# Kernel tuning notes

Hardware: AMD Instinct MI355X
Metric: run time of the kernel (lower is better)

The kernel has to match this reference:

```python
import jax, jax.numpy as jnp
import numpy as np

B, CI, H, W = 16, 32, 224, 224
CO, K, STRIDE = 32, 3, 1


def setup_inputs() -> dict:
    key = jax.random.key(0)
    k1, k2, k3 = jax.random.split(key, 3)
    x = jax.random.normal(k1, (B, CI, H, W), dtype=jnp.float32)
    weights = jax.random.normal(k2, (CO, CI, K, K), dtype=jnp.float32)
    bias = jax.random.normal(k3, (CO,), dtype=jnp.float32)
    return {"x": x, "weights": weights, "bias": bias}


def reference(x, weights, bias):
    # Faithful to HandmadeConv2D with padding=0, stride=1: a VALID
    # cross-correlation (the torch code never actually pads x) plus bias.
    out = jax.lax.conv_general_dilated(
        x, weights,
        window_strides=(STRIDE, STRIDE),
        padding="VALID",
        dimension_numbers=("NCHW", "OIHW", "NCHW"),
    )
    return out + bias[None, :, None, None]
```

## Files before the change

kernel.cpp:

```cpp
#include <hip/hip_runtime.h>
#include <hip/hip_bf16.h>

#define B_   16
#define CI_  32
#define H_   224
#define W_   224
#define CO_  32
#define OH_  222
#define OW_  222
#define HW_  (H_*W_)
#define K_   288

#define OWTW   64
#define PXT_   66
#define NPAIR  33
#define RING   10
#define SLABB  (PXT_*CI_*2)
#define CHROWS 20
#define NCHUNK 12
#define NBLK   (NCHUNK*4*B_)

typedef __attribute__((ext_vector_type(8))) short short8;
typedef __attribute__((ext_vector_type(4))) float float4v;
typedef float float4u __attribute__((ext_vector_type(4), aligned(4)));

__device__ __forceinline__ unsigned swz(unsigned L) {
    return L ^ (((L >> 7) & 7u) << 4);
}

__device__ __forceinline__ int wrap10(int v) {
    if (v >= 20) return v - 20;
    if (v >= 10) return v - 10;
    return v;
}

__global__ void wprep(const float* __restrict__ w, unsigned short* __restrict__ wbf) {
    int idx = blockIdx.x * 256 + threadIdx.x;
    if (idx >= CO_ * K_) return;
    int co  = idx / K_;
    int rem = idx - co * K_;
    int ci  = rem / 9;
    int g   = rem - ci * 9;
    unsigned int u = __float_as_uint(w[idx]);
    u = u + 0x7FFFu + ((u >> 16) & 1u);
    wbf[co * K_ + g * 32 + ci] = (unsigned short)(u >> 16);
}

__device__ __forceinline__ void load_pair(const float* __restrict__ xp, int c, float2* f2) {
    if (c + 1 < W_) {
#pragma unroll
        for (int i = 0; i < 32; ++i)
            f2[i] = *(const float2*)&xp[(size_t)i * HW_ + c];
    } else {
#pragma unroll
        for (int i = 0; i < 32; ++i) {
            float v = xp[(size_t)i * HW_ + (W_ - 1)];
            f2[i] = make_float2(v, v);
        }
    }
}

__device__ __forceinline__ void cvt_write_pair(unsigned short* Xs, int slot, int j,
                                               const float2* f2) {
    union { short8 s8[8]; __hip_bfloat162 h2[32]; } u;
#pragma unroll
    for (int i = 0; i < 16; ++i) {
        u.h2[i]      = __float22bfloat162_rn(make_float2(f2[2*i].x, f2[2*i+1].x));
        u.h2[16 + i] = __float22bfloat162_rn(make_float2(f2[2*i].y, f2[2*i+1].y));
    }
    const unsigned base = (unsigned)(slot * NPAIR + j) * 128u;
#pragma unroll
    for (int k = 0; k < 8; ++k)
        *(short8*)((char*)Xs + swz(base + (unsigned)k * 16u)) = u.s8[k];
}

__global__ __launch_bounds__(256, 3) void conv_fused(
    const float* __restrict__ x, const unsigned short* __restrict__ wbf,
    const float* __restrict__ bias, float* __restrict__ out)
{
    __shared__ unsigned short Xs[RING * PXT_ * CI_];

    const int t   = threadIdx.x;
    const int bid = blockIdx.x;
    const int xcd   = bid & 7;
    const int owt   = (bid >> 3) & 3;
    const int gid   = (bid >> 5) * 8 + xcd;
    const int b     = gid / NCHUNK;
    const int chunk = gid - b * NCHUNK;
    const int r0    = chunk * CHROWS;
    const int ow0   = owt * OWTW;
    const int NS    = min(5, (OH_ - r0 + 3) >> 2);

    const int lane = t & 63, wv = t >> 6;
    const int i16  = lane & 15, quad = lane >> 4;

    const float* xb = x + (size_t)b * CI_ * HW_;

    float2 f2[32];

    if (t < 6 * NPAIR) {
        const int tr = t / NPAIR, j = t - tr * NPAIR;
        int gr = r0 + tr; if (gr > H_ - 1) gr = H_ - 1;
        load_pair(xb + (size_t)gr * W_, ow0 + 2 * j, f2);
        cvt_write_pair(Xs, tr, j, f2);
    }
    __syncthreads();

    const float bv0 = bias[i16];
    const float bv1 = bias[16 + i16];
    const unsigned short* wr0 = wbf + (size_t)i16 * K_;
    const unsigned short* wr1 = wbf + (size_t)(16 + i16) * K_;

    const int s_tr = t / NPAIR;
    const int s_j  = t - s_tr * NPAIR;
    const int s_c  = ow0 + 2 * s_j;

    for (int s = 0; s < NS; ++s) {
        const bool pref = (t < 4 * NPAIR) && (s + 1 < NS);
        int slotW = 0;
        if (pref) {
            const int gr0 = r0 + 4 * s + 6 + s_tr;
            slotW = wrap10(4 * s + 6 + s_tr);
            const int gr = gr0 > H_ - 1 ? H_ - 1 : gr0;
            load_pair(xb + (size_t)gr * W_, s_c, f2);
        }
        __builtin_amdgcn_sched_barrier(0);

        const int oh = r0 + 4 * s + wv;
        if (oh < OH_) {
            float4v acc[4][2] = {};
            const int sl0 = 4 * s + wv;
#pragma unroll
            for (int g = 0; g < 9; ++g) {
                const int kh = g / 3, kw = g - kh * 3;
                const int sl = wrap10(sl0 + kh);
                const short8 b0 = *(const short8*)&wr0[g * 32 + quad * 8];
                const short8 b1 = *(const short8*)&wr1[g * 32 + quad * 8];
                const unsigned rowbase = (unsigned)(sl * SLABB) + (unsigned)quad * 16u;
#pragma unroll
                for (int ot = 0; ot < 4; ++ot) {
                    const unsigned L = rowbase + (unsigned)(ot * 16 + i16 + kw) * 64u;
                    const short8 a = *(const short8*)((const char*)Xs + swz(L));
                    acc[ot][0] = __builtin_amdgcn_mfma_f32_16x16x32_bf16(a, b0, acc[ot][0], 0, 0, 0);
                    acc[ot][1] = __builtin_amdgcn_mfma_f32_16x16x32_bf16(a, b1, acc[ot][1], 0, 0, 0);
                }
            }
            const size_t o0 = ((size_t)(b * CO_ + i16) * OH_ + oh) * (size_t)OW_;
            const size_t o1 = ((size_t)(b * CO_ + 16 + i16) * OH_ + oh) * (size_t)OW_;
#pragma unroll
            for (int ot = 0; ot < 4; ++ot) {
                const int owq = ow0 + ot * 16 + quad * 4;
                float4u v0 = { acc[ot][0][0] + bv0, acc[ot][0][1] + bv0,
                               acc[ot][0][2] + bv0, acc[ot][0][3] + bv0 };
                float4u v1 = { acc[ot][1][0] + bv1, acc[ot][1][1] + bv1,
                               acc[ot][1][2] + bv1, acc[ot][1][3] + bv1 };
                if (owq + 3 < OW_) {
                    *(float4u*)&out[o0 + owq] = v0;
                    *(float4u*)&out[o1 + owq] = v1;
                } else {
#pragma unroll
                    for (int r = 0; r < 4; ++r)
                        if (owq + r < OW_) {
                            out[o0 + owq + r] = acc[ot][0][r] + bv0;
                            out[o1 + owq + r] = acc[ot][1][r] + bv1;
                        }
                }
            }
        }

        if (pref) cvt_write_pair(Xs, slotW, s_j, f2);
        __syncthreads();
    }
}

extern "C" void kernel_launch(void* const* d_in, const int* in_sizes, int n_in,
                              void* d_out, int out_size, void* d_ws, size_t ws_size,
                              hipStream_t stream) {
    const float* x    = (const float*)d_in[0];
    const float* w    = (const float*)d_in[1];
    const float* bias = (const float*)d_in[2];
    float* out        = (float*)d_out;
    unsigned short* wbf = (unsigned short*)d_ws;

    wprep<<<(CO_ * K_ + 255) / 256, 256, 0, stream>>>(w, wbf);
    conv_fused<<<dim3(NBLK), 256, 0, stream>>>(x, wbf, bias, out);
}
```

Measured before the change: 233.9 us.

## Double threads per block, splitting channel loads and output tiles across waves

Moves from 256 to 512 threads per block. Each loader thread now fetches half of the 32 input channels (16 float2 values instead of 32), which halves register pressure from the prefetch buffer. Each of the 8 waves computes two 16-column output tiles instead of four. The goal is more memory-level parallelism and more resident waves (launch bounds 512,6) to hide global load latency. The cost is that per-wave weight fragment loads are duplicated and there are more threads per barrier.

```diff
diff --git a/kernel.cpp b/kernel.cpp
--- a/kernel.cpp
+++ b/kernel.cpp
@@ -19,6 +19,8 @@
 #define CHROWS 20
 #define NCHUNK 12
 #define NBLK   (NCHUNK*4*B_)
+#define STG    264
+#define PRO    396
 
 typedef __attribute__((ext_vector_type(8))) short short8;
 typedef __attribute__((ext_vector_type(4))) float float4v;
@@ -46,35 +48,38 @@
     wbf[co * K_ + g * 32 + ci] = (unsigned short)(u >> 16);
 }
 
-__device__ __forceinline__ void load_pair(const float* __restrict__ xp, int c, float2* f2) {
+__device__ __forceinline__ void load_half(const float* __restrict__ xp, int c, int h,
+                                          float2* f2) {
+    const float* p = xp + (size_t)(h * 16) * HW_;
     if (c + 1 < W_) {
 #pragma unroll
-        for (int i = 0; i < 32; ++i)
-            f2[i] = *(const float2*)&xp[(size_t)i * HW_ + c];
+        for (int i = 0; i < 16; ++i)
+            f2[i] = *(const float2*)&p[(size_t)i * HW_ + c];
     } else {
 #pragma unroll
-        for (int i = 0; i < 32; ++i) {
-            float v = xp[(size_t)i * HW_ + (W_ - 1)];
+        for (int i = 0; i < 16; ++i) {
+            float v = p[(size_t)i * HW_ + (W_ - 1)];
             f2[i] = make_float2(v, v);
         }
     }
 }
 
-__device__ __forceinline__ void cvt_write_pair(unsigned short* Xs, int slot, int j,
+__device__ __forceinline__ void cvt_write_half(unsigned short* Xs, int slot, int j, int h,
                                                const float2* f2) {
-    union { short8 s8[8]; __hip_bfloat162 h2[32]; } u;
-#pragma unroll
-    for (int i = 0; i < 16; ++i) {
-        u.h2[i]      = __float22bfloat162_rn(make_float2(f2[2*i].x, f2[2*i+1].x));
-        u.h2[16 + i] = __float22bfloat162_rn(make_float2(f2[2*i].y, f2[2*i+1].y));
+    union { short8 s8[4]; __hip_bfloat162 h2[16]; } u;
+#pragma unroll
+    for (int i = 0; i < 8; ++i) {
+        u.h2[i]     = __float22bfloat162_rn(make_float2(f2[2*i].x, f2[2*i+1].x));
+        u.h2[8 + i] = __float22bfloat162_rn(make_float2(f2[2*i].y, f2[2*i+1].y));
     }
     const unsigned base = (unsigned)(slot * NPAIR + j) * 128u;
-#pragma unroll
-    for (int k = 0; k < 8; ++k)
-        *(short8*)((char*)Xs + swz(base + (unsigned)k * 16u)) = u.s8[k];
-}
-
-__global__ __launch_bounds__(256, 3) void conv_fused(
+    *(short8*)((char*)Xs + swz(base + (unsigned)(2*h)     * 16u)) = u.s8[0];
+    *(short8*)((char*)Xs + swz(base + (unsigned)(2*h + 1) * 16u)) = u.s8[1];
+    *(short8*)((char*)Xs + swz(base + (unsigned)(4 + 2*h) * 16u)) = u.s8[2];
+    *(short8*)((char*)Xs + swz(base + (unsigned)(5 + 2*h) * 16u)) = u.s8[3];
+}
+
+__global__ __launch_bounds__(512, 6) void conv_fused(
     const float* __restrict__ x, const unsigned short* __restrict__ wbf,
     const float* __restrict__ bias, float* __restrict__ out)
 {
@@ -96,13 +101,15 @@
 
     const float* xb = x + (size_t)b * CI_ * HW_;
 
-    float2 f2[32];
-
-    if (t < 6 * NPAIR) {
-        const int tr = t / NPAIR, j = t - tr * NPAIR;
+    float2 f2[16];
+
+    if (t < PRO) {
+        const int h  = t & 1;
+        const int pj = t >> 1;
+        const int tr = pj / NPAIR, j = pj - tr * NPAIR;
         int gr = r0 + tr; if (gr > H_ - 1) gr = H_ - 1;
-        load_pair(xb + (size_t)gr * W_, ow0 + 2 * j, f2);
-        cvt_write_pair(Xs, tr, j, f2);
+        load_half(xb + (size_t)gr * W_, ow0 + 2 * j, h, f2);
+        cvt_write_half(Xs, tr, j, h, f2);
     }
     __syncthreads();
 
@@ -111,25 +118,30 @@
     const unsigned short* wr0 = wbf + (size_t)i16 * K_;
     const unsigned short* wr1 = wbf + (size_t)(16 + i16) * K_;
 
-    const int s_tr = t / NPAIR;
-    const int s_j  = t - s_tr * NPAIR;
+    const int s_h  = t & 1;
+    const int s_pj = t >> 1;
+    const int s_tr = s_pj / NPAIR;
+    const int s_j  = s_pj - s_tr * NPAIR;
     const int s_c  = ow0 + 2 * s_j;
 
+    const int row = wv >> 1;
+    const int oth = wv & 1;
+
     for (int s = 0; s < NS; ++s) {
-        const bool pref = (t < 4 * NPAIR) && (s + 1 < NS);
+        const bool pref = (t < STG) && (s + 1 < NS);
         int slotW = 0;
         if (pref) {
             const int gr0 = r0 + 4 * s + 6 + s_tr;
             slotW = wrap10(4 * s + 6 + s_tr);
             const int gr = gr0 > H_ - 1 ? H_ - 1 : gr0;
-            load_pair(xb + (size_t)gr * W_, s_c, f2);
+            load_half(xb + (size_t)gr * W_, s_c, s_h, f2);
         }
         __builtin_amdgcn_sched_barrier(0);
 
-        const int oh = r0 + 4 * s + wv;
+        const int oh = r0 + 4 * s + row;
         if (oh < OH_) {
-            float4v acc[4][2] = {};
-            const int sl0 = 4 * s + wv;
+            float4v acc[2][2] = {};
+            const int sl0 = 4 * s + row;
 #pragma unroll
             for (int g = 0; g < 9; ++g) {
                 const int kh = g / 3, kw = g - kh * 3;
@@ -138,22 +150,24 @@
                 const short8 b1 = *(const short8*)&wr1[g * 32 + quad * 8];
                 const unsigned rowbase = (unsigned)(sl * SLABB) + (unsigned)quad * 16u;
 #pragma unroll
-                for (int ot = 0; ot < 4; ++ot) {
+                for (int oti = 0; oti < 2; ++oti) {
+                    const int ot = 2 * oth + oti;
                     const unsigned L = rowbase + (unsigned)(ot * 16 + i16 + kw) * 64u;
                     const short8 a = *(const short8*)((const char*)Xs + swz(L));
-                    acc[ot][0] = __builtin_amdgcn_mfma_f32_16x16x32_bf16(a, b0, acc[ot][0], 0, 0, 0);
-                    acc[ot][1] = __builtin_amdgcn_mfma_f32_16x16x32_bf16(a, b1, acc[ot][1], 0, 0, 0);
+                    acc[oti][0] = __builtin_amdgcn_mfma_f32_16x16x32_bf16(a, b0, acc[oti][0], 0, 0, 0);
+                    acc[oti][1] = __builtin_amdgcn_mfma_f32_16x16x32_bf16(a, b1, acc[oti][1], 0, 0, 0);
                 }
             }
             const size_t o0 = ((size_t)(b * CO_ + i16) * OH_ + oh) * (size_t)OW_;
             const size_t o1 = ((size_t)(b * CO_ + 16 + i16) * OH_ + oh) * (size_t)OW_;
 #pragma unroll
-            for (int ot = 0; ot < 4; ++ot) {
+            for (int oti = 0; oti < 2; ++oti) {
+                const int ot  = 2 * oth + oti;
                 const int owq = ow0 + ot * 16 + quad * 4;
-                float4u v0 = { acc[ot][0][0] + bv0, acc[ot][0][1] + bv0,
-                               acc[ot][0][2] + bv0, acc[ot][0][3] + bv0 };
-                float4u v1 = { acc[ot][1][0] + bv1, acc[ot][1][1] + bv1,
-                               acc[ot][1][2] + bv1, acc[ot][1][3] + bv1 };
+                float4u v0 = { acc[oti][0][0] + bv0, acc[oti][0][1] + bv0,
+                               acc[oti][0][2] + bv0, acc[oti][0][3] + bv0 };
+                float4u v1 = { acc[oti][1][0] + bv1, acc[oti][1][1] + bv1,
+                               acc[oti][1][2] + bv1, acc[oti][1][3] + bv1 };
                 if (owq + 3 < OW_) {
                     *(float4u*)&out[o0 + owq] = v0;
                     *(float4u*)&out[o1 + owq] = v1;
@@ -161,14 +175,14 @@
 #pragma unroll
                     for (int r = 0; r < 4; ++r)
                         if (owq + r < OW_) {
-                            out[o0 + owq + r] = acc[ot][0][r] + bv0;
-                            out[o1 + owq + r] = acc[ot][1][r] + bv1;
+                            out[o0 + owq + r] = acc[oti][0][r] + bv0;
+                            out[o1 + owq + r] = acc[oti][1][r] + bv1;
                         }
                 }
             }
         }
 
-        if (pref) cvt_write_pair(Xs, slotW, s_j, f2);
+        if (pref) cvt_write_half(Xs, slotW, s_j, s_h, f2);
         __syncthreads();
     }
 }
@@ -183,5 +197,5 @@
     unsigned short* wbf = (unsigned short*)d_ws;
 
     wprep<<<(CO_ * K_ + 255) / 256, 256, 0, stream>>>(w, wbf);
-    conv_fused<<<dim3(NBLK), 256, 0, stream>>>(x, wbf, bias, out);
-}
+    conv_fused<<<dim3(NBLK), 512, 0, stream>>>(x, wbf, bias, out);
+}
```

Result: slower. 286.8 us (+22.6%).
